# Optimization experiments

Measured on AMD Instinct MI355X. Metric: run time of the kernel, lower is better.

The kernel has to match this reference:

```python
import jax, jax.numpy as jnp
import numpy as np

IN_FEATURES = 48
OUT_FEATURES = 64
ALPHA = 0.2  # LeakyReLU negative slope
NUM_INTENT = 16
N = 8192


def setup_inputs() -> dict:
    key = jax.random.key(0)
    k1, k2, k3, k4, k5 = jax.random.split(key, 5)
    # Xavier-uniform-ish params (exact init doesn't matter for correctness testing)
    W = jax.random.uniform(k1, (IN_FEATURES, OUT_FEATURES), jnp.float32, -0.3, 0.3)
    a = jax.random.uniform(k2, (2 * OUT_FEATURES, 1), jnp.float32, -0.3, 0.3)
    intent_interaction = jax.random.normal(k3, (NUM_INTENT, NUM_INTENT), jnp.float32) * 0.1
    intent_alpha = jnp.asarray(0.1, jnp.float32)
    inp = jax.random.normal(k4, (N, IN_FEATURES), jnp.float32)
    adj = jnp.ones((N, N), jnp.float32)  # unused by the math, kept for signature fidelity
    intent_labels = jax.random.randint(k5, (N,), 0, NUM_INTENT, jnp.int64 if jax.config.jax_enable_x64 else jnp.int32)
    return {"input": inp, "adj": adj, "W": W, "a": a,
            "intent_interaction": intent_interaction, "intent_alpha": intent_alpha,
            "intent_labels": intent_labels}


def reference(input, adj, W, a, intent_interaction, intent_alpha, intent_labels):
    h = input @ W                       # [N, F]
    F_ = h.shape[1]
    a1 = a[:F_, 0]                      # source part of attention vector
    a2 = a[F_:, 0]                      # target part
    # e[i,j] = leakyrelu(a1.h_i + a2.h_j) without materializing [N,N,2F]
    s1 = h @ a1                         # [N]
    s2 = h @ a2                         # [N]
    spatial_e = jax.nn.leaky_relu(s1[:, None] + s2[None, :], negative_slope=ALPHA)
    # intent bias: gather from interaction matrix, no python loops
    idx = jnp.clip(intent_labels - 1, 0, NUM_INTENT - 1)
    intent_bias = intent_interaction[idx[:, None], idx[None, :]]  # [N, N]
    total_e = spatial_e + intent_alpha * intent_bias
    # NOTE: original softmaxes over dim=0 (columns) and does NOT mask with adj
    attention = jax.nn.softmax(total_e, axis=0)
    h_prime = attention @ h             # [N, F]
    return jax.nn.elu(h_prime)          # concat=True path
```

## Files before the change

kernel.cpp:

```cpp
#include <hip/hip_runtime.h>

#define NN 8192
#define FF 64
#define INF 48
#define NC 16
#define CAP 2048
#define LOG2E 1.4426950408889634f

__device__ __forceinline__ float fexp2(float x) { return __builtin_amdgcn_exp2f(x); }
__device__ __forceinline__ float elu(float v) { return v > 0.f ? v : __expf(v) - 1.f; }

__global__ __launch_bounds__(256) void k1(const float* __restrict__ in,
                                          const float* __restrict__ W,
                                          const float* __restrict__ a,
                                          const int* __restrict__ labels,
                                          float* __restrict__ h,
                                          float* __restrict__ s1L,
                                          float* __restrict__ s2L,
                                          int* __restrict__ ci) {
  __shared__ float sIn[4][INF];
  int t = threadIdx.x;
  int w = t >> 6, lane = t & 63;
  int i = blockIdx.x * 4 + w;
  if (lane < INF) sIn[w][lane] = in[i * INF + lane];
  __syncthreads();
  float acc = 0.f;
#pragma unroll
  for (int k = 0; k < INF; k++) acc += sIn[w][k] * W[k * FF + lane];
  h[i * FF + lane] = acc;
  float v1 = acc * a[lane];
  float v2 = acc * a[FF + lane];
#pragma unroll
  for (int off = 32; off > 0; off >>= 1) {
    v1 += __shfl_xor(v1, off, 64);
    v2 += __shfl_xor(v2, off, 64);
  }
  if (lane == 0) {
    s1L[i] = v1 * LOG2E;
    s2L[i] = v2 * LOG2E;
    int c = labels[i] - 1;
    ci[i] = c < 0 ? 0 : (c > 15 ? 15 : c);
  }
}

__global__ __launch_bounds__(1024) void k2(const float* __restrict__ s1L,
                                           const float* __restrict__ s2L,
                                           const int* __restrict__ ci,
                                           int* __restrict__ offG,
                                           float* __restrict__ s1s,
                                           float* __restrict__ sufA,
                                           float* __restrict__ preB,
                                           float* __restrict__ s2s,
                                           int* __restrict__ perm2,
                                           float* __restrict__ ea2,
                                           float* __restrict__ eb2) {
  __shared__ int wcnt[16][16];
  __shared__ int tot[16];
  __shared__ int offL[17];
  __shared__ int idxL[CAP];
  __shared__ float key[CAP];
  __shared__ int pay[CAP];
  __shared__ float exA[CAP];
  __shared__ float exB[CAP];
  __shared__ float wred[32];
  __shared__ float wexA[17], wexB[17];
  __shared__ int gcnt;
  int t = threadIdx.x;
  int wv = t >> 6, lane = t & 63;
  int myc = blockIdx.x;
  unsigned long long lower = (1ULL << lane) - 1ULL;
  int c8[8];
#pragma unroll
  for (int k = 0; k < 8; k++) c8[k] = ci[wv * 512 + k * 64 + lane];
  if (t == 0) gcnt = 0;
#pragma unroll 1
  for (int cls = 0; cls < 16; cls++) {
    int run = 0;
#pragma unroll
    for (int k = 0; k < 8; k++) run += __popcll(__ballot(c8[k] == cls));
    if (lane == 0) wcnt[wv][cls] = run;
  }
  __syncthreads();
  if (t < 16) {
    int s = 0;
#pragma unroll
    for (int w = 0; w < 16; w++) s += wcnt[w][t];
    tot[t] = s;
  }
  __syncthreads();
  if (t == 0) {
    int s = 0;
    for (int c = 0; c < 16; c++) { offL[c] = s; s += tot[c]; }
    offL[16] = s;
  }
  __syncthreads();
  if (myc == 0 && t < 17) offG[t] = offL[t];
  int moff = offL[myc], msz = tot[myc];
  int offE = moff + myc;
#pragma unroll
  for (int k = 0; k < 8; k++) {
    bool is = (c8[k] == myc);
    unsigned long long m = __ballot(is);
    int cnt = __popcll(m);
    int base = 0;
    if (lane == 0 && cnt) base = atomicAdd(&gcnt, cnt);
    base = __shfl(base, 0, 64);
    if (is) idxL[base + __popcll(m & lower)] = wv * 512 + k * 64 + lane;
  }
  __syncthreads();
  bool fast = (msz <= 1024);
  if (fast) {
    float v = (t < msz) ? s1L[idxL[t]] : 3.0e38f;
#pragma unroll
    for (int kk = 2; kk <= 64; kk <<= 1) {
#pragma unroll
      for (int jj = kk >> 1; jj > 0; jj >>= 1) {
        bool sel = ((t & kk) == 0) == ((t & jj) == 0);
        float pv = __shfl_xor(v, jj, 64);
        v = sel ? fminf(v, pv) : fmaxf(v, pv);
      }
    }
    key[t] = v;
    __syncthreads();
    for (int kk = 128; kk <= 1024; kk <<= 1) {
      for (int jj = kk >> 1; jj >= 64; jj >>= 1) {
        int l = t ^ jj;
        if (l > t) {
          float av = key[t], bv = key[l];
          if ((av > bv) == ((t & kk) == 0)) { key[t] = bv; key[l] = av; }
        }
        __syncthreads();
      }
      v = key[t];
      bool up = ((t & kk) == 0);
#pragma unroll
      for (int jj = 32; jj > 0; jj >>= 1) {
        bool sel = up == ((t & jj) == 0);
        float pv = __shfl_xor(v, jj, 64);
        v = sel ? fminf(v, pv) : fmaxf(v, pv);
      }
      key[t] = v;
      __syncthreads();
    }
  } else {
    for (int m = t; m < CAP; m += 1024) key[m] = (m < msz) ? s1L[idxL[m]] : 3.0e38f;
    __syncthreads();
    for (int kk = 2; kk <= CAP; kk <<= 1) {
      for (int jj = kk >> 1; jj > 0; jj >>= 1) {
        for (int i = t; i < CAP; i += 1024) {
          int l = i ^ jj;
          if (l > i) {
            float av = key[i], bv = key[l];
            if ((av > bv) == ((i & kk) == 0)) { key[i] = bv; key[l] = av; }
          }
        }
        __syncthreads();
      }
    }
  }
  for (int m = t; m < CAP; m += 1024) {
    bool in = m < msz;
    float kv = in ? key[m] : 0.f;
    if (in) s1s[moff + m] = kv;
    exA[m] = in ? fexp2(kv) : 0.f;
    exB[m] = in ? fexp2(0.2f * kv) : 0.f;
  }
  __syncthreads();
  float v0 = exA[2 * t], v1 = exA[2 * t + 1];
  float u0 = exB[2 * t], u1 = exB[2 * t + 1];
  float ts = v0 + v1, us = u0 + u1;
  float tsi = ts, usi = us;
#pragma unroll
  for (int d = 1; d < 64; d <<= 1) {
    float nA = __shfl_up(tsi, d, 64);
    float nB = __shfl_up(usi, d, 64);
    if (lane >= d) { tsi += nA; usi += nB; }
  }
  if (lane == 63) { wred[wv] = tsi; wred[16 + wv] = usi; }
  __syncthreads();
  if (t == 0) {
    float sA = 0.f, sB = 0.f;
    for (int w = 0; w < 16; w++) { wexA[w] = sA; wexB[w] = sB; sA += wred[w]; sB += wred[16 + w]; }
    wexA[16] = sA; wexB[16] = sB;
  }
  __syncthreads();
  float eAr = wexA[wv] + (tsi - ts);
  float eBr = wexB[wv] + (usi - us);
  exA[2 * t] = eAr; exA[2 * t + 1] = eAr + v0;
  exB[2 * t] = eBr; exB[2 * t + 1] = eBr + u0;
  __syncthreads();
  float totA = wexA[16];
  for (int k = t; k <= msz; k += 1024) {
    sufA[offE + k] = totA - exA[k];
    preB[offE + k] = exB[k];
  }
  if (fast) {
    float v2 = (t < msz) ? s2L[idxL[t]] : 3.0e38f;
    int pj = (t < msz) ? idxL[t] : -1;
#pragma unroll
    for (int kk = 2; kk <= 64; kk <<= 1) {
#pragma unroll
      for (int jj = kk >> 1; jj > 0; jj >>= 1) {
        bool sel = ((t & kk) == 0) == ((t & jj) == 0);
        float pv = __shfl_xor(v2, jj, 64);
        int pp = __shfl_xor(pj, jj, 64);
        bool take = sel ? (pv < v2) : (pv > v2);
        if (take) { v2 = pv; pj = pp; }
      }
    }
    key[t] = v2;
    pay[t] = pj;
    __syncthreads();
    for (int kk = 128; kk <= 1024; kk <<= 1) {
      for (int jj = kk >> 1; jj >= 64; jj >>= 1) {
        int l = t ^ jj;
        if (l > t) {
          float av = key[t], bv = key[l];
          if ((av > bv) == ((t & kk) == 0)) {
            key[t] = bv; key[l] = av;
            int pt = pay[t]; pay[t] = pay[l]; pay[l] = pt;
          }
        }
        __syncthreads();
      }
      v2 = key[t];
      pj = pay[t];
      bool up = ((t & kk) == 0);
#pragma unroll
      for (int jj = 32; jj > 0; jj >>= 1) {
        bool sel = up == ((t & jj) == 0);
        float pv = __shfl_xor(v2, jj, 64);
        int pp = __shfl_xor(pj, jj, 64);
        bool take = sel ? (pv < v2) : (pv > v2);
        if (take) { v2 = pv; pj = pp; }
      }
      key[t] = v2;
      pay[t] = pj;
      __syncthreads();
    }
  } else {
    for (int m = t; m < CAP; m += 1024) {
      bool in = m < msz;
      key[m] = in ? s2L[idxL[m]] : 3.0e38f;
      pay[m] = in ? idxL[m] : -1;
    }
    __syncthreads();
    for (int kk = 2; kk <= CAP; kk <<= 1) {
      for (int jj = kk >> 1; jj > 0; jj >>= 1) {
        for (int i = t; i < CAP; i += 1024) {
          int l = i ^ jj;
          if (l > i) {
            float av = key[i], bv = key[l];
            if ((av > bv) == ((i & kk) == 0)) {
              key[i] = bv; key[l] = av;
              int pt = pay[i]; pay[i] = pay[l]; pay[l] = pt;
            }
          }
        }
        __syncthreads();
      }
    }
  }
  for (int m = t; m < msz; m += 1024) {
    float kv = key[m];
    s2s[moff + m] = kv;
    perm2[moff + m] = pay[m];
    ea2[moff + m] = fexp2(kv);
    eb2[moff + m] = fexp2(0.2f * kv);
  }
}

__global__ __launch_bounds__(256) void k3(const float* __restrict__ s2L,
                                          const int* __restrict__ ci,
                                          const int* __restrict__ offG,
                                          const float* __restrict__ s1s,
                                          const float* __restrict__ sufA,
                                          const float* __restrict__ preB,
                                          const float* __restrict__ Bmat,
                                          const float* __restrict__ alphap,
                                          float* __restrict__ Dinv) {
  __shared__ float EBT[256];
  __shared__ int offL[17];
  int t = threadIdx.x;
  EBT[t] = __expf(alphap[0] * Bmat[t]);
  if (t < 17) offL[t] = offG[t];
  __syncthreads();
  int c = t & 15, il = t >> 4;
  int o = offL[c], n = offL[c + 1] - o;
  int j = blockIdx.x * 16 + il;
  float s2v = s2L[j];
  int cj = ci[j];
  float keyv = -s2v;
  int lo = 0, len = n;
  while (len > 0) {
    int half = len >> 1;
    int mid = lo + half;
    if (s1s[o + mid] <= keyv) { lo = mid + 1; len -= half + 1; }
    else len = half;
  }
  int b = o + c + lo;
  float term = EBT[c * 16 + cj] * fmaf(fexp2(s2v), sufA[b], fexp2(0.2f * s2v) * preB[b]);
#pragma unroll
  for (int d = 1; d < 16; d <<= 1) term += __shfl_xor(term, d, 64);
  if (c == 0) Dinv[j] = 1.0f / term;
}

__global__ __launch_bounds__(256) void k3b(const int* __restrict__ perm2,
                                           const float* __restrict__ ea2,
                                           const float* __restrict__ eb2,
                                           const float* __restrict__ Dinv,
                                           const float* __restrict__ h,
                                           float* __restrict__ hpA,
                                           float* __restrict__ hpB) {
  int t = threadIdx.x;
  int wv = t >> 6, f = t & 63;
  int base = blockIdx.x * 16 + wv * 4;
#pragma unroll
  for (int r = 0; r < 4; r++) {
    int pos = base + r;
    int j = perm2[pos];
    float g = Dinv[j];
    float ea = ea2[pos], eb = eb2[pos];
    float hv = h[j * FF + f];
    hpA[(size_t)pos * FF + f] = ea * g * hv;
    hpB[(size_t)pos * FF + f] = eb * g * hv;
  }
}

__global__ __launch_bounds__(1024) void k4(const int* __restrict__ offG,
                                           const float* __restrict__ hpA,
                                           const float* __restrict__ hpB,
                                           float* __restrict__ sufG1,
                                           float* __restrict__ preG2) {
  __shared__ float ps[16][64];
  __shared__ int offL[17];
  int t = threadIdx.x;
  int wv = t >> 6, f = t & 63;
  if (t < 17) offL[t] = offG[t];
  __syncthreads();
  int cls = blockIdx.x;
  int o = offL[cls], sz = offL[cls + 1] - o, oE = o + cls;
  int dir = wv >> 3, w8 = wv & 7;
  int L = (sz + 7) >> 3;
  int m0 = w8 * L;
  if (m0 > sz) m0 = sz;
  int m1 = m0 + L;
  if (m1 > sz) m1 = sz;
  float acc = 0.f;
  if (dir == 0) {
#pragma unroll 4
    for (int m = m0; m < m1; m++) acc += hpA[(size_t)(o + m) * FF + f];
  } else {
#pragma unroll 4
    for (int m = m0; m < m1; m++) acc += hpB[(size_t)(o + m) * FF + f];
  }
  ps[wv][f] = acc;
  __syncthreads();
  if (dir == 0) {
    float run = 0.f;
    for (int w = w8 + 1; w < 8; w++) run += ps[w][f];
#pragma unroll 4
    for (int m = m1 - 1; m >= m0; m--) {
      run += hpA[(size_t)(o + m) * FF + f];
      sufG1[(size_t)(oE + m) * FF + f] = run;
    }
    if (wv == 0) sufG1[(size_t)(oE + sz) * FF + f] = 0.f;
  } else {
    float run = 0.f;
    for (int w = 0; w < w8; w++) run += ps[8 + w][f];
#pragma unroll 4
    for (int m = m0; m < m1; m++) {
      preG2[(size_t)(oE + m) * FF + f] = run;
      run += hpB[(size_t)(o + m) * FF + f];
    }
    if (w8 == 7) preG2[(size_t)(oE + sz) * FF + f] = run;
  }
}

__global__ __launch_bounds__(256) void k5(const float* __restrict__ s1L,
                                          const int* __restrict__ ci,
                                          const int* __restrict__ offG,
                                          const float* __restrict__ s2s,
                                          const float* __restrict__ sufG1,
                                          const float* __restrict__ preG2,
                                          const float* __restrict__ Bmat,
                                          const float* __restrict__ alphap,
                                          float* __restrict__ out) {
  __shared__ float EBT[256];
  __shared__ int offL[17];
  int t = threadIdx.x;
  EBT[t] = __expf(alphap[0] * Bmat[t]);
  if (t < 17) offL[t] = offG[t];
  __syncthreads();
  int wv = t >> 6, l = t & 63;
  int i = blockIdx.x * 4 + wv;
  float s1v = s1L[i];
  int ai = ci[i];
  int lo = 0;
  if (l < 16) {
    int o = offL[l], len = offL[l + 1] - o;
    float keyv = -s1v;
    while (len > 0) {
      int half = len >> 1;
      int mid = lo + half;
      if (s2s[o + mid] <= keyv) { lo = mid + 1; len -= half + 1; }
      else len = half;
    }
  }
  float e1 = fexp2(s1v), e1b = fexp2(0.2f * s1v);
  float acc = 0.f;
#pragma unroll
  for (int c = 0; c < NC; c++) {
    int k = __shfl(lo, c, 64);
    int base = (offL[c] + c + k) * FF + l;
    acc = fmaf(EBT[ai * 16 + c], fmaf(e1, sufG1[base], e1b * preG2[base]), acc);
  }
  out[i * FF + l] = elu(acc);
}

extern "C" void kernel_launch(void* const* d_in, const int* in_sizes, int n_in,
                              void* d_out, int out_size, void* d_ws, size_t ws_size,
                              hipStream_t stream) {
  const float* in = (const float*)d_in[0];
  const float* W = (const float*)d_in[2];
  const float* a = (const float*)d_in[3];
  const float* Bmat = (const float*)d_in[4];
  const float* alpha = (const float*)d_in[5];
  const int* labels = (const int*)d_in[6];
  float* out = (float*)d_out;

  float* ws = (float*)d_ws;
  float* h = ws;
  float* s1L = h + 524288;
  float* s2L = s1L + 8192;
  int* ci = (int*)(s2L + 8192);
  int* offG = ci + 8192;
  float* s1s = (float*)(offG + 32);
  float* sufA = s1s + 8192;
  float* preB = sufA + 8224;
  float* s2s = preB + 8224;
  int* perm2 = (int*)(s2s + 8192);
  float* ea2 = (float*)(perm2 + 8192);
  float* eb2 = ea2 + 8192;
  float* Dinv = eb2 + 8192;
  float* hpA = Dinv + 8192;
  float* hpB = hpA + 524288;
  float* sufG1 = hpB + 524288;
  float* preG2 = sufG1 + 8224 * 64;

  k1<<<2048, 256, 0, stream>>>(in, W, a, labels, h, s1L, s2L, ci);
  k2<<<16, 1024, 0, stream>>>(s1L, s2L, ci, offG, s1s, sufA, preB, s2s, perm2, ea2, eb2);
  k3<<<512, 256, 0, stream>>>(s2L, ci, offG, s1s, sufA, preB, Bmat, alpha, Dinv);
  k3b<<<512, 256, 0, stream>>>(perm2, ea2, eb2, Dinv, h, hpA, hpB);
  k4<<<16, 1024, 0, stream>>>(offG, hpA, hpB, sufG1, preG2);
  k5<<<2048, 256, 0, stream>>>(s1L, ci, offG, s2s, sufG1, preG2, Bmat, alpha, out);
}
```

Measured before the change: 412.0 us.

## Split per-class sorts and scans across two blocks and fuse k3 with k3b

The per-class sort kernel now launches two blocks per class, so the s1 and s2 sorts and their follow-up work run in parallel instead of back to back. The slow path for large classes becomes a two-elements-per-thread bitonic sort that uses shuffles for the inner stages. The denominator kernel is fused with the weighting kernel: it walks rows in perm2 order, keeps Dinv in shared memory and writes hpA/hpB directly, which drops the Dinv round trip and one launch. The prefix-scan kernel also runs two blocks per class, one per direction, with 16 waves each. Both halves of k2 redo the class counting, so that work is duplicated.

```diff
diff --git a/kernel.cpp b/kernel.cpp
--- a/kernel.cpp
+++ b/kernel.cpp
@@ -67,7 +67,8 @@
   __shared__ int gcnt;
   int t = threadIdx.x;
   int wv = t >> 6, lane = t & 63;
-  int myc = blockIdx.x;
+  int myc = blockIdx.x >> 1;
+  int half = blockIdx.x & 1;
   unsigned long long lower = (1ULL << lane) - 1ULL;
   int c8[8];
 #pragma unroll
@@ -94,7 +95,7 @@
     offL[16] = s;
   }
   __syncthreads();
-  if (myc == 0 && t < 17) offG[t] = offL[t];
+  if (blockIdx.x == 0 && t < 17) offG[t] = offL[t];
   int moff = offL[myc], msz = tot[myc];
   int offE = moff + myc;
 #pragma unroll
@@ -108,188 +109,267 @@
     if (is) idxL[base + __popcll(m & lower)] = wv * 512 + k * 64 + lane;
   }
   __syncthreads();
+  const float* src = (half == 0) ? s1L : s2L;
   bool fast = (msz <= 1024);
-  if (fast) {
-    float v = (t < msz) ? s1L[idxL[t]] : 3.0e38f;
-#pragma unroll
-    for (int kk = 2; kk <= 64; kk <<= 1) {
-#pragma unroll
-      for (int jj = kk >> 1; jj > 0; jj >>= 1) {
-        bool sel = ((t & kk) == 0) == ((t & jj) == 0);
-        float pv = __shfl_xor(v, jj, 64);
-        v = sel ? fminf(v, pv) : fmaxf(v, pv);
-      }
-    }
-    key[t] = v;
-    __syncthreads();
-    for (int kk = 128; kk <= 1024; kk <<= 1) {
-      for (int jj = kk >> 1; jj >= 64; jj >>= 1) {
-        int l = t ^ jj;
-        if (l > t) {
-          float av = key[t], bv = key[l];
-          if ((av > bv) == ((t & kk) == 0)) { key[t] = bv; key[l] = av; }
-        }
-        __syncthreads();
-      }
-      v = key[t];
-      bool up = ((t & kk) == 0);
-#pragma unroll
-      for (int jj = 32; jj > 0; jj >>= 1) {
-        bool sel = up == ((t & jj) == 0);
-        float pv = __shfl_xor(v, jj, 64);
-        v = sel ? fminf(v, pv) : fmaxf(v, pv);
+  if (half == 0) {
+    if (fast) {
+      float v = (t < msz) ? src[idxL[t]] : 3.0e38f;
+#pragma unroll
+      for (int kk = 2; kk <= 64; kk <<= 1) {
+#pragma unroll
+        for (int jj = kk >> 1; jj > 0; jj >>= 1) {
+          bool sel = ((t & kk) == 0) == ((t & jj) == 0);
+          float pv = __shfl_xor(v, jj, 64);
+          v = sel ? fminf(v, pv) : fmaxf(v, pv);
+        }
       }
       key[t] = v;
       __syncthreads();
-    }
-  } else {
-    for (int m = t; m < CAP; m += 1024) key[m] = (m < msz) ? s1L[idxL[m]] : 3.0e38f;
-    __syncthreads();
-    for (int kk = 2; kk <= CAP; kk <<= 1) {
-      for (int jj = kk >> 1; jj > 0; jj >>= 1) {
-        for (int i = t; i < CAP; i += 1024) {
-          int l = i ^ jj;
-          if (l > i) {
-            float av = key[i], bv = key[l];
-            if ((av > bv) == ((i & kk) == 0)) { key[i] = bv; key[l] = av; }
+      for (int kk = 128; kk <= 1024; kk <<= 1) {
+        for (int jj = kk >> 1; jj >= 64; jj >>= 1) {
+          int l = t ^ jj;
+          if (l > t) {
+            float av = key[t], bv = key[l];
+            if ((av > bv) == ((t & kk) == 0)) { key[t] = bv; key[l] = av; }
           }
-        }
+          __syncthreads();
+        }
+        v = key[t];
+        bool up = ((t & kk) == 0);
+#pragma unroll
+        for (int jj = 32; jj > 0; jj >>= 1) {
+          bool sel = up == ((t & jj) == 0);
+          float pv = __shfl_xor(v, jj, 64);
+          v = sel ? fminf(v, pv) : fmaxf(v, pv);
+        }
+        key[t] = v;
         __syncthreads();
       }
-    }
-  }
-  for (int m = t; m < CAP; m += 1024) {
-    bool in = m < msz;
-    float kv = in ? key[m] : 0.f;
-    if (in) s1s[moff + m] = kv;
-    exA[m] = in ? fexp2(kv) : 0.f;
-    exB[m] = in ? fexp2(0.2f * kv) : 0.f;
-  }
-  __syncthreads();
-  float v0 = exA[2 * t], v1 = exA[2 * t + 1];
-  float u0 = exB[2 * t], u1 = exB[2 * t + 1];
-  float ts = v0 + v1, us = u0 + u1;
-  float tsi = ts, usi = us;
-#pragma unroll
-  for (int d = 1; d < 64; d <<= 1) {
-    float nA = __shfl_up(tsi, d, 64);
-    float nB = __shfl_up(usi, d, 64);
-    if (lane >= d) { tsi += nA; usi += nB; }
-  }
-  if (lane == 63) { wred[wv] = tsi; wred[16 + wv] = usi; }
-  __syncthreads();
-  if (t == 0) {
-    float sA = 0.f, sB = 0.f;
-    for (int w = 0; w < 16; w++) { wexA[w] = sA; wexB[w] = sB; sA += wred[w]; sB += wred[16 + w]; }
-    wexA[16] = sA; wexB[16] = sB;
-  }
-  __syncthreads();
-  float eAr = wexA[wv] + (tsi - ts);
-  float eBr = wexB[wv] + (usi - us);
-  exA[2 * t] = eAr; exA[2 * t + 1] = eAr + v0;
-  exB[2 * t] = eBr; exB[2 * t + 1] = eBr + u0;
-  __syncthreads();
-  float totA = wexA[16];
-  for (int k = t; k <= msz; k += 1024) {
-    sufA[offE + k] = totA - exA[k];
-    preB[offE + k] = exB[k];
-  }
-  if (fast) {
-    float v2 = (t < msz) ? s2L[idxL[t]] : 3.0e38f;
-    int pj = (t < msz) ? idxL[t] : -1;
-#pragma unroll
-    for (int kk = 2; kk <= 64; kk <<= 1) {
-#pragma unroll
-      for (int jj = kk >> 1; jj > 0; jj >>= 1) {
-        bool sel = ((t & kk) == 0) == ((t & jj) == 0);
-        float pv = __shfl_xor(v2, jj, 64);
-        int pp = __shfl_xor(pj, jj, 64);
-        bool take = sel ? (pv < v2) : (pv > v2);
-        if (take) { v2 = pv; pj = pp; }
-      }
-    }
-    key[t] = v2;
-    pay[t] = pj;
-    __syncthreads();
-    for (int kk = 128; kk <= 1024; kk <<= 1) {
-      for (int jj = kk >> 1; jj >= 64; jj >>= 1) {
-        int l = t ^ jj;
-        if (l > t) {
-          float av = key[t], bv = key[l];
-          if ((av > bv) == ((t & kk) == 0)) {
-            key[t] = bv; key[l] = av;
-            int pt = pay[t]; pay[t] = pay[l]; pay[l] = pt;
+    } else {
+      key[t] = (t < msz) ? src[idxL[t]] : 3.0e38f;
+      key[t + 1024] = (t + 1024 < msz) ? src[idxL[t + 1024]] : 3.0e38f;
+      __syncthreads();
+      float v0 = key[t], v1 = key[t + 1024];
+#pragma unroll
+      for (int kk = 2; kk <= 64; kk <<= 1) {
+#pragma unroll
+        for (int jj = kk >> 1; jj > 0; jj >>= 1) {
+          bool sel = ((t & kk) == 0) == ((t & jj) == 0);
+          float p0 = __shfl_xor(v0, jj, 64);
+          float p1 = __shfl_xor(v1, jj, 64);
+          v0 = sel ? fminf(v0, p0) : fmaxf(v0, p0);
+          v1 = sel ? fminf(v1, p1) : fmaxf(v1, p1);
+        }
+      }
+      key[t] = v0; key[t + 1024] = v1;
+      __syncthreads();
+      for (int kk = 128; kk <= 2048; kk <<= 1) {
+        for (int jj = kk >> 1; jj >= 64; jj >>= 1) {
+#pragma unroll
+          for (int e2 = 0; e2 < 2; e2++) {
+            int e = t + e2 * 1024;
+            int l = e ^ jj;
+            if (l > e) {
+              float av = key[e], bv = key[l];
+              if ((av > bv) == ((e & kk) == 0)) { key[e] = bv; key[l] = av; }
+            }
           }
-        }
+          __syncthreads();
+        }
+        v0 = key[t]; v1 = key[t + 1024];
+        bool up0 = ((t & kk) == 0);
+        bool up1 = (((t + 1024) & kk) == 0);
+#pragma unroll
+        for (int jj = 32; jj > 0; jj >>= 1) {
+          bool s2b = ((t & jj) == 0);
+          float p0 = __shfl_xor(v0, jj, 64);
+          float p1 = __shfl_xor(v1, jj, 64);
+          v0 = (up0 == s2b) ? fminf(v0, p0) : fmaxf(v0, p0);
+          v1 = (up1 == s2b) ? fminf(v1, p1) : fmaxf(v1, p1);
+        }
+        key[t] = v0; key[t + 1024] = v1;
         __syncthreads();
       }
-      v2 = key[t];
-      pj = pay[t];
-      bool up = ((t & kk) == 0);
-#pragma unroll
-      for (int jj = 32; jj > 0; jj >>= 1) {
-        bool sel = up == ((t & jj) == 0);
-        float pv = __shfl_xor(v2, jj, 64);
-        int pp = __shfl_xor(pj, jj, 64);
-        bool take = sel ? (pv < v2) : (pv > v2);
-        if (take) { v2 = pv; pj = pp; }
-      }
-      key[t] = v2;
-      pay[t] = pj;
-      __syncthreads();
-    }
-  } else {
+    }
     for (int m = t; m < CAP; m += 1024) {
       bool in = m < msz;
-      key[m] = in ? s2L[idxL[m]] : 3.0e38f;
-      pay[m] = in ? idxL[m] : -1;
+      float kv = in ? key[m] : 0.f;
+      if (in) s1s[moff + m] = kv;
+      exA[m] = in ? fexp2(kv) : 0.f;
+      exB[m] = in ? fexp2(0.2f * kv) : 0.f;
     }
     __syncthreads();
-    for (int kk = 2; kk <= CAP; kk <<= 1) {
-      for (int jj = kk >> 1; jj > 0; jj >>= 1) {
-        for (int i = t; i < CAP; i += 1024) {
-          int l = i ^ jj;
-          if (l > i) {
-            float av = key[i], bv = key[l];
-            if ((av > bv) == ((i & kk) == 0)) {
-              key[i] = bv; key[l] = av;
-              int pt = pay[i]; pay[i] = pay[l]; pay[l] = pt;
+    float v0 = exA[2 * t], v1 = exA[2 * t + 1];
+    float u0 = exB[2 * t], u1 = exB[2 * t + 1];
+    float ts = v0 + v1, us = u0 + u1;
+    float tsi = ts, usi = us;
+#pragma unroll
+    for (int d = 1; d < 64; d <<= 1) {
+      float nA = __shfl_up(tsi, d, 64);
+      float nB = __shfl_up(usi, d, 64);
+      if (lane >= d) { tsi += nA; usi += nB; }
+    }
+    if (lane == 63) { wred[wv] = tsi; wred[16 + wv] = usi; }
+    __syncthreads();
+    if (t == 0) {
+      float sA = 0.f, sB = 0.f;
+      for (int w = 0; w < 16; w++) { wexA[w] = sA; wexB[w] = sB; sA += wred[w]; sB += wred[16 + w]; }
+      wexA[16] = sA; wexB[16] = sB;
+    }
+    __syncthreads();
+    float eAr = wexA[wv] + (tsi - ts);
+    float eBr = wexB[wv] + (usi - us);
+    exA[2 * t] = eAr; exA[2 * t + 1] = eAr + v0;
+    exB[2 * t] = eBr; exB[2 * t + 1] = eBr + u0;
+    __syncthreads();
+    float totA = wexA[16];
+    for (int k = t; k <= msz; k += 1024) {
+      sufA[offE + k] = totA - exA[k];
+      preB[offE + k] = exB[k];
+    }
+  } else {
+    if (fast) {
+      float v = (t < msz) ? src[idxL[t]] : 3.0e38f;
+      int pj = (t < msz) ? idxL[t] : -1;
+#pragma unroll
+      for (int kk = 2; kk <= 64; kk <<= 1) {
+#pragma unroll
+        for (int jj = kk >> 1; jj > 0; jj >>= 1) {
+          bool sel = ((t & kk) == 0) == ((t & jj) == 0);
+          float pv = __shfl_xor(v, jj, 64);
+          int pp = __shfl_xor(pj, jj, 64);
+          bool take = sel ? (pv < v) : (pv > v);
+          if (take) { v = pv; pj = pp; }
+        }
+      }
+      key[t] = v; pay[t] = pj;
+      __syncthreads();
+      for (int kk = 128; kk <= 1024; kk <<= 1) {
+        for (int jj = kk >> 1; jj >= 64; jj >>= 1) {
+          int l = t ^ jj;
+          if (l > t) {
+            float av = key[t], bv = key[l];
+            if ((av > bv) == ((t & kk) == 0)) {
+              key[t] = bv; key[l] = av;
+              int pt = pay[t]; pay[t] = pay[l]; pay[l] = pt;
             }
           }
-        }
+          __syncthreads();
+        }
+        v = key[t]; pj = pay[t];
+        bool up = ((t & kk) == 0);
+#pragma unroll
+        for (int jj = 32; jj > 0; jj >>= 1) {
+          bool sel = up == ((t & jj) == 0);
+          float pv = __shfl_xor(v, jj, 64);
+          int pp = __shfl_xor(pj, jj, 64);
+          bool take = sel ? (pv < v) : (pv > v);
+          if (take) { v = pv; pj = pp; }
+        }
+        key[t] = v; pay[t] = pj;
         __syncthreads();
       }
-    }
-  }
-  for (int m = t; m < msz; m += 1024) {
-    float kv = key[m];
-    s2s[moff + m] = kv;
-    perm2[moff + m] = pay[m];
-    ea2[moff + m] = fexp2(kv);
-    eb2[moff + m] = fexp2(0.2f * kv);
+    } else {
+      key[t] = (t < msz) ? src[idxL[t]] : 3.0e38f;
+      pay[t] = (t < msz) ? idxL[t] : -1;
+      key[t + 1024] = (t + 1024 < msz) ? src[idxL[t + 1024]] : 3.0e38f;
+      pay[t + 1024] = (t + 1024 < msz) ? idxL[t + 1024] : -1;
+      __syncthreads();
+      float v0 = key[t], v1 = key[t + 1024];
+      int p0i = pay[t], p1i = pay[t + 1024];
+#pragma unroll
+      for (int kk = 2; kk <= 64; kk <<= 1) {
+#pragma unroll
+        for (int jj = kk >> 1; jj > 0; jj >>= 1) {
+          bool sel = ((t & kk) == 0) == ((t & jj) == 0);
+          float q0 = __shfl_xor(v0, jj, 64);
+          int r0 = __shfl_xor(p0i, jj, 64);
+          float q1 = __shfl_xor(v1, jj, 64);
+          int r1 = __shfl_xor(p1i, jj, 64);
+          bool tk0 = sel ? (q0 < v0) : (q0 > v0);
+          bool tk1 = sel ? (q1 < v1) : (q1 > v1);
+          if (tk0) { v0 = q0; p0i = r0; }
+          if (tk1) { v1 = q1; p1i = r1; }
+        }
+      }
+      key[t] = v0; pay[t] = p0i;
+      key[t + 1024] = v1; pay[t + 1024] = p1i;
+      __syncthreads();
+      for (int kk = 128; kk <= 2048; kk <<= 1) {
+        for (int jj = kk >> 1; jj >= 64; jj >>= 1) {
+#pragma unroll
+          for (int e2 = 0; e2 < 2; e2++) {
+            int e = t + e2 * 1024;
+            int l = e ^ jj;
+            if (l > e) {
+              float av = key[e], bv = key[l];
+              if ((av > bv) == ((e & kk) == 0)) {
+                key[e] = bv; key[l] = av;
+                int pt = pay[e]; pay[e] = pay[l]; pay[l] = pt;
+              }
+            }
+          }
+          __syncthreads();
+        }
+        v0 = key[t]; v1 = key[t + 1024];
+        p0i = pay[t]; p1i = pay[t + 1024];
+        bool up0 = ((t & kk) == 0);
+        bool up1 = (((t + 1024) & kk) == 0);
+#pragma unroll
+        for (int jj = 32; jj > 0; jj >>= 1) {
+          bool s2b = ((t & jj) == 0);
+          float q0 = __shfl_xor(v0, jj, 64);
+          int r0 = __shfl_xor(p0i, jj, 64);
+          float q1 = __shfl_xor(v1, jj, 64);
+          int r1 = __shfl_xor(p1i, jj, 64);
+          bool tk0 = (up0 == s2b) ? (q0 < v0) : (q0 > v0);
+          bool tk1 = (up1 == s2b) ? (q1 < v1) : (q1 > v1);
+          if (tk0) { v0 = q0; p0i = r0; }
+          if (tk1) { v1 = q1; p1i = r1; }
+        }
+        key[t] = v0; pay[t] = p0i;
+        key[t + 1024] = v1; pay[t + 1024] = p1i;
+        __syncthreads();
+      }
+    }
+    for (int m = t; m < msz; m += 1024) {
+      float kv = key[m];
+      s2s[moff + m] = kv;
+      perm2[moff + m] = pay[m];
+      ea2[moff + m] = fexp2(kv);
+      eb2[moff + m] = fexp2(0.2f * kv);
+    }
   }
 }
 
-__global__ __launch_bounds__(256) void k3(const float* __restrict__ s2L,
-                                          const int* __restrict__ ci,
-                                          const int* __restrict__ offG,
-                                          const float* __restrict__ s1s,
-                                          const float* __restrict__ sufA,
-                                          const float* __restrict__ preB,
-                                          const float* __restrict__ Bmat,
-                                          const float* __restrict__ alphap,
-                                          float* __restrict__ Dinv) {
+__global__ __launch_bounds__(256) void k3p(const float* __restrict__ s2L,
+                                           const int* __restrict__ ci,
+                                           const int* __restrict__ offG,
+                                           const float* __restrict__ s1s,
+                                           const float* __restrict__ sufA,
+                                           const float* __restrict__ preB,
+                                           const int* __restrict__ perm2,
+                                           const float* __restrict__ ea2,
+                                           const float* __restrict__ eb2,
+                                           const float* __restrict__ h,
+                                           const float* __restrict__ Bmat,
+                                           const float* __restrict__ alphap,
+                                           float* __restrict__ hpA,
+                                           float* __restrict__ hpB) {
   __shared__ float EBT[256];
   __shared__ int offL[17];
+  __shared__ float DinvL[16];
+  __shared__ int jL[16];
   int t = threadIdx.x;
   EBT[t] = __expf(alphap[0] * Bmat[t]);
   if (t < 17) offL[t] = offG[t];
   __syncthreads();
-  int c = t & 15, il = t >> 4;
-  int o = offL[c], n = offL[c + 1] - o;
-  int j = blockIdx.x * 16 + il;
+  int il = t >> 4, c = t & 15;
+  int pos0 = blockIdx.x * 16;
+  int j = perm2[pos0 + il];
   float s2v = s2L[j];
   int cj = ci[j];
+  int o = offL[c], n = offL[c + 1] - o;
   float keyv = -s2v;
   int lo = 0, len = n;
   while (len > 0) {
@@ -302,28 +382,18 @@
   float term = EBT[c * 16 + cj] * fmaf(fexp2(s2v), sufA[b], fexp2(0.2f * s2v) * preB[b]);
 #pragma unroll
   for (int d = 1; d < 16; d <<= 1) term += __shfl_xor(term, d, 64);
-  if (c == 0) Dinv[j] = 1.0f / term;
-}
-
-__global__ __launch_bounds__(256) void k3b(const int* __restrict__ perm2,
-                                           const float* __restrict__ ea2,
-                                           const float* __restrict__ eb2,
-                                           const float* __restrict__ Dinv,
-                                           const float* __restrict__ h,
-                                           float* __restrict__ hpA,
-                                           float* __restrict__ hpB) {
-  int t = threadIdx.x;
-  int wv = t >> 6, f = t & 63;
-  int base = blockIdx.x * 16 + wv * 4;
+  if (c == 0) { DinvL[il] = 1.0f / term; jL[il] = j; }
+  __syncthreads();
+  int wv = t >> 6, lane = t & 63;
 #pragma unroll
   for (int r = 0; r < 4; r++) {
-    int pos = base + r;
-    int j = perm2[pos];
-    float g = Dinv[j];
-    float ea = ea2[pos], eb = eb2[pos];
-    float hv = h[j * FF + f];
-    hpA[(size_t)pos * FF + f] = ea * g * hv;
-    hpB[(size_t)pos * FF + f] = eb * g * hv;
+    int rr = wv * 4 + r;
+    int pp = pos0 + rr;
+    float g = DinvL[rr];
+    int jj = jL[rr];
+    float hv = h[jj * FF + lane];
+    hpA[(size_t)pp * FF + lane] = ea2[pp] * g * hv;
+    hpB[(size_t)pp * FF + lane] = eb2[pp] * g * hv;
   }
 }
 
@@ -338,42 +408,37 @@
   int wv = t >> 6, f = t & 63;
   if (t < 17) offL[t] = offG[t];
   __syncthreads();
-  int cls = blockIdx.x;
+  int cls = blockIdx.x >> 1, dir = blockIdx.x & 1;
   int o = offL[cls], sz = offL[cls + 1] - o, oE = o + cls;
-  int dir = wv >> 3, w8 = wv & 7;
-  int L = (sz + 7) >> 3;
-  int m0 = w8 * L;
+  int L = (sz + 15) >> 4;
+  int m0 = wv * L;
   if (m0 > sz) m0 = sz;
   int m1 = m0 + L;
   if (m1 > sz) m1 = sz;
+  const float* src = dir ? hpB : hpA;
   float acc = 0.f;
-  if (dir == 0) {
 #pragma unroll 4
-    for (int m = m0; m < m1; m++) acc += hpA[(size_t)(o + m) * FF + f];
-  } else {
-#pragma unroll 4
-    for (int m = m0; m < m1; m++) acc += hpB[(size_t)(o + m) * FF + f];
-  }
+  for (int m = m0; m < m1; m++) acc += src[(size_t)(o + m) * FF + f];
   ps[wv][f] = acc;
   __syncthreads();
   if (dir == 0) {
     float run = 0.f;
-    for (int w = w8 + 1; w < 8; w++) run += ps[w][f];
+    for (int w = wv + 1; w < 16; w++) run += ps[w][f];
 #pragma unroll 4
     for (int m = m1 - 1; m >= m0; m--) {
-      run += hpA[(size_t)(o + m) * FF + f];
+      run += src[(size_t)(o + m) * FF + f];
       sufG1[(size_t)(oE + m) * FF + f] = run;
     }
     if (wv == 0) sufG1[(size_t)(oE + sz) * FF + f] = 0.f;
   } else {
     float run = 0.f;
-    for (int w = 0; w < w8; w++) run += ps[8 + w][f];
+    for (int w = 0; w < wv; w++) run += ps[w][f];
 #pragma unroll 4
     for (int m = m0; m < m1; m++) {
       preG2[(size_t)(oE + m) * FF + f] = run;
-      run += hpB[(size_t)(o + m) * FF + f];
-    }
-    if (w8 == 7) preG2[(size_t)(oE + sz) * FF + f] = run;
+      run += src[(size_t)(o + m) * FF + f];
+    }
+    if (wv == 15) preG2[(size_t)(oE + sz) * FF + f] = run;
   }
 }
 
@@ -442,16 +507,14 @@
   int* perm2 = (int*)(s2s + 8192);
   float* ea2 = (float*)(perm2 + 8192);
   float* eb2 = ea2 + 8192;
-  float* Dinv = eb2 + 8192;
-  float* hpA = Dinv + 8192;
+  float* hpA = eb2 + 8192;
   float* hpB = hpA + 524288;
   float* sufG1 = hpB + 524288;
   float* preG2 = sufG1 + 8224 * 64;
 
   k1<<<2048, 256, 0, stream>>>(in, W, a, labels, h, s1L, s2L, ci);
-  k2<<<16, 1024, 0, stream>>>(s1L, s2L, ci, offG, s1s, sufA, preB, s2s, perm2, ea2, eb2);
-  k3<<<512, 256, 0, stream>>>(s2L, ci, offG, s1s, sufA, preB, Bmat, alpha, Dinv);
-  k3b<<<512, 256, 0, stream>>>(perm2, ea2, eb2, Dinv, h, hpA, hpB);
-  k4<<<16, 1024, 0, stream>>>(offG, hpA, hpB, sufG1, preG2);
+  k2<<<32, 1024, 0, stream>>>(s1L, s2L, ci, offG, s1s, sufA, preB, s2s, perm2, ea2, eb2);
+  k3p<<<512, 256, 0, stream>>>(s2L, ci, offG, s1s, sufA, preB, perm2, ea2, eb2, h, Bmat, alpha, hpA, hpB);
+  k4<<<32, 1024, 0, stream>>>(offG, hpA, hpB, sufG1, preG2);
   k5<<<2048, 256, 0, stream>>>(s1L, ci, offG, s2s, sufG1, preG2, Bmat, alpha, out);
 }
```

After: 357.7 us. -13.2%, faster.
